# Optimization experiments

Measured on AMD Instinct MI355X. Metric: run time of the kernel, lower is better.

Reference implementation:

```python
import jax, jax.numpy as jnp
import numpy as np

B, N, DEG = 8, 8192, 16
E = B * N * DEG
K1 = 2458  # ceil(0.3*8192)
K2 = 738   # ceil(0.3*2458)
NUM_CLASSES = 10


def gat(x, src, dst, emask, W, a_s, a_d, bias):
    # PyG GATConv with add_self_loops=True, negative_slope=0.2, concat heads
    n = x.shape[0]
    H, F = a_s.shape
    xp = (x @ W).reshape(n, H, F)                      # [n,H,F]
    al_s = (xp * a_s).sum(-1)                          # [n,H]
    al_d = (xp * a_d).sum(-1)
    loops = jnp.arange(n, dtype=src.dtype)
    s2 = jnp.concatenate([src, loops])
    d2 = jnp.concatenate([dst, loops])
    m2 = jnp.concatenate([emask, jnp.ones(n, bool)])
    e = jax.nn.leaky_relu(al_s[s2] + al_d[d2], 0.2)    # [E+n,H]
    e = jnp.where(m2[:, None], e, -1e9)
    emax = jax.ops.segment_max(e, d2, num_segments=n)
    ex = jnp.where(m2[:, None], jnp.exp(e - emax[d2]), 0.0)
    den = jax.ops.segment_sum(ex, d2, num_segments=n)
    msg = ex[:, :, None] * xp[s2]                      # [E+n,H,F]
    out = jax.ops.segment_sum(msg, d2, num_segments=n) / den[:, :, None]
    return out.reshape(n, H * F) + bias


def inorm(x):
    # PyG InstanceNorm (affine=False): per-graph per-channel normalization
    xb = x.reshape(B, -1, x.shape[-1])
    mu = xb.mean(1, keepdims=True)
    var = ((xb - mu) ** 2).mean(1, keepdims=True)
    return ((xb - mu) / jnp.sqrt(var + 1e-5)).reshape(x.shape)


def topk_pool(x, src, dst, emask, p, k):
    # TopKPooling: score = tanh(x.p/|p|), keep top-k per graph, scale x by score
    n_tot = x.shape[0]
    n = n_tot // B
    score = jnp.tanh((x @ p) / jnp.linalg.norm(p))
    sv, si = jax.lax.top_k(score.reshape(B, n), k)     # [B,k]
    xg = jnp.take_along_axis(x.reshape(B, n, -1), si[:, :, None], axis=1)
    xnew = (xg * sv[:, :, None]).reshape(B * k, -1)
    perm = (si + (jnp.arange(B) * n)[:, None]).reshape(-1)
    newid = jnp.full(n_tot, -1, dtype=src.dtype).at[perm].set(
        jnp.arange(B * k, dtype=src.dtype))
    ns, nd = newid[src], newid[dst]
    m = emask & (ns >= 0) & (nd >= 0)
    return xnew, jnp.maximum(ns, 0), jnp.maximum(nd, 0), m


def setup_inputs() -> dict:
    key = jax.random.key(0)
    ks = jax.random.split(key, 32)
    pos = jax.random.normal(ks[0], (B * N, 3), jnp.float32)
    offs = jnp.repeat(jnp.arange(B, dtype=jnp.int32) * N, N * DEG)
    src = jax.random.randint(ks[1], (E,), 0, N, jnp.int32) + offs
    dst = jax.random.randint(ks[2], (E,), 0, N, jnp.int32) + offs

    def lin(k, fi, fo):
        return jax.random.normal(k, (fi, fo), jnp.float32) * (1.0 / np.sqrt(fi))

    d = dict(pos=pos, src=src, dst=dst)
    d['W1'] = lin(ks[3], 3, 32);   d['a_s1'] = jax.random.normal(ks[4], (2, 16)) * 0.2
    d['a_d1'] = jax.random.normal(ks[5], (2, 16)) * 0.2
    d['b1'] = jnp.zeros((32,));    d['p1'] = jax.random.normal(ks[6], (32,))
    d['W2'] = lin(ks[7], 32, 128); d['a_s2'] = jax.random.normal(ks[8], (2, 64)) * 0.2
    d['a_d2'] = jax.random.normal(ks[9], (2, 64)) * 0.2
    d['b2'] = jnp.zeros((128,));   d['p2'] = jax.random.normal(ks[10], (128,))
    d['W3'] = lin(ks[11], 128, 256); d['a_s3'] = jax.random.normal(ks[12], (1, 256)) * 0.1
    d['a_d3'] = jax.random.normal(ks[13], (1, 256)) * 0.1
    d['b3'] = jnp.zeros((256,))
    d['gw1'] = lin(ks[14], 256, 64);  d['gb1'] = jnp.zeros((64,))
    d['gw2'] = lin(ks[15], 64, 1);    d['gb2'] = jnp.zeros((1,))
    d['aw'] = lin(ks[16], 256, 256);  d['ab'] = jnp.zeros((256,))
    d['w1'] = lin(ks[17], 256, 512);  d['bb1'] = jnp.zeros((512,))
    d['w2'] = lin(ks[18], 512, 128);  d['bb2'] = jnp.zeros((128,))
    d['w3'] = lin(ks[19], 128, NUM_CLASSES); d['bb3'] = jnp.zeros((NUM_CLASSES,))
    return d


def reference(pos, src, dst, W1, a_s1, a_d1, b1, p1, W2, a_s2, a_d2, b2, p2,
              W3, a_s3, a_d3, b3, gw1, gb1, gw2, gb2, aw, ab,
              w1, bb1, w2, bb2, w3, bb3):
    emask = jnp.ones(src.shape[0], bool)
    x = gat(pos, src, dst, emask, W1, a_s1, a_d1, b1)
    x = jax.nn.elu(inorm(x))
    x, src, dst, emask = topk_pool(x, src, dst, emask, p1, K1)
    x = gat(x, src, dst, emask, W2, a_s2, a_d2, b2)
    x = jax.nn.elu(inorm(x))
    x, src, dst, emask = topk_pool(x, src, dst, emask, p2, K2)
    x = gat(x, src, dst, emask, W3, a_s3, a_d3, b3)
    x = jax.nn.elu(inorm(x))
    # GlobalAttention: gate_nn = Linear(256,64)+ELU+Linear(64,1); nn = Linear+ELU
    gate = jax.nn.elu(x @ gw1 + gb1) @ gw2 + gb2       # [M,1]
    h = jax.nn.elu(x @ aw + ab)                        # [M,256]
    a = jax.nn.softmax(gate.reshape(B, K2, 1), axis=1)
    g = (a * h.reshape(B, K2, 256)).sum(1)             # [B,256]
    z = jax.nn.elu(g @ w1 + bb1)   # dropout inactive in eval
    z = jax.nn.elu(z @ w2 + bb2)
    z = z @ w3 + bb3
    return jax.nn.log_softmax(z, axis=1)
```

## Files before the change

### kernel.cpp

```cpp
#include <hip/hip_runtime.h>
#include <cstdint>
#include <cstddef>

#define DI __device__ __forceinline__

namespace pk {

constexpr int NB1 = 65536;
constexpr int NE  = 1048576;
constexpr int BG  = 8;
constexpr int NPG1 = 8192;
constexpr int EPG1 = NE/BG;
constexpr int KP1 = 2458;
constexpr int KP2 = 738;
constexpr int NN2 = BG*KP1;
constexpr int NN3 = BG*KP2;
constexpr int REG2 = 16384;
constexpr int REG3 = 4096;
constexpr int CAP2 = BG*REG2;
constexpr int CAP3 = BG*REG3;
constexpr int CPB1 = 16;
constexpr int NTILE = 32;
constexpr int BKT = 5120;

DI float lrelu(float x){ return x > 0.f ? x : 0.2f*x; }
DI float eluf(float x){ return x > 0.f ? x : expf(x) - 1.f; }

DI int swz_block(){
  int nb = gridDim.x, b = blockIdx.x;
  if((nb & 7) == 0) return (b & 7)*(nb >> 3) + (b >> 3);
  return b;
}

__global__ __launch_bounds__(1024) void k_s1_front(
    const float* __restrict__ pos, const float* __restrict__ W,
    const float* __restrict__ as_, const float* __restrict__ ad_,
    float* __restrict__ xp, float* __restrict__ als, float* __restrict__ ald,
    const int* __restrict__ se, const int* __restrict__ de,
    int* __restrict__ part, int* __restrict__ bcur, int* __restrict__ bpk){
  __shared__ int h[NPG1];
  __shared__ int hbase[NTILE];
  __shared__ int hc[NTILE];
  int tid = threadIdx.x;
  if(blockIdx.x < 64){
    int i = blockIdx.x*1024 + tid;
    float p0=pos[3*i], p1=pos[3*i+1], p2=pos[3*i+2];
    float row[32];
#pragma unroll
    for(int c=0;c<32;c++) row[c] = p0*W[c] + p1*W[32+c] + p2*W[64+c];
    float s0=0.f,d0=0.f,s1=0.f,d1=0.f;
#pragma unroll
    for(int f=0;f<16;f++){
      s0 += row[f]*as_[f];        d0 += row[f]*ad_[f];
      s1 += row[16+f]*as_[16+f];  d1 += row[16+f]*ad_[16+f];
    }
    float4* o = reinterpret_cast<float4*>(xp + (size_t)i*32);
#pragma unroll
    for(int q=0;q<8;q++) o[q] = make_float4(row[4*q],row[4*q+1],row[4*q+2],row[4*q+3]);
    als[2*i]=s0; als[2*i+1]=s1; ald[2*i]=d0; ald[2*i+1]=d1;
    return;
  }
  int bb = blockIdx.x - 64;
  int g = bb & 7, t = bb >> 3;
  for(int i=tid;i<NPG1;i+=1024) h[i]=0;
  __syncthreads();
  const int4* de4 = (const int4*)(de + g*EPG1 + t*(EPG1/CPB1));
  const int4* se4 = (const int4*)(se + g*EPG1 + t*(EPG1/CPB1));
  int lo = g*NPG1;
  int4 dv[2], sv[2];
#pragma unroll
  for(int j=0;j<2;j++){ dv[j]=de4[j*1024+tid]; sv[j]=se4[j*1024+tid]; }
  int dl[8], sl[8];
#pragma unroll
  for(int j=0;j<2;j++){
    dl[4*j+0]=dv[j].x-lo; dl[4*j+1]=dv[j].y-lo; dl[4*j+2]=dv[j].z-lo; dl[4*j+3]=dv[j].w-lo;
    sl[4*j+0]=sv[j].x-lo; sl[4*j+1]=sv[j].y-lo; sl[4*j+2]=sv[j].z-lo; sl[4*j+3]=sv[j].w-lo;
  }
#pragma unroll
  for(int q=0;q<8;q++) atomicAdd(&h[dl[q]],1);
  __syncthreads();
  if(tid < NTILE){
    int ssum = 0;
    for(int i=0;i<256;i++) ssum += h[tid*256+i];
    hbase[tid] = atomicAdd(&bcur[g*NTILE+tid], ssum);
    hc[tid] = 0;
  }
  int* pp = part + (size_t)(g*CPB1+t)*NPG1;
  for(int i=tid;i<NPG1;i+=1024) pp[i]=h[i];
  __syncthreads();
#pragma unroll
  for(int q=0;q<8;q++){
    int tt = dl[q] >> 8;
    int p = atomicAdd(&hc[tt],1) + hbase[tt];
    bpk[(size_t)(g*NTILE+tt)*BKT + p] = (sl[q]<<13) | dl[q];
  }
}

__global__ __launch_bounds__(1024) void k_scan1(
    const int* __restrict__ part, int* __restrict__ cnt,
    int* __restrict__ rowptr){
  __shared__ int wsum[16];
  int g = blockIdx.x;
  int tid = threadIdx.x, lane = tid & 63, w = tid >> 6;
  constexpr int PER = NPG1/1024;
  int base = g*NPG1;
  int i0 = tid*PER;
  int v[PER]; int s = 0;
#pragma unroll
  for(int j=0;j<PER;j++){
    int i = i0+j;
    int x = 0;
#pragma unroll
    for(int p=0;p<CPB1;p++) x += part[(size_t)(g*CPB1+p)*NPG1 + i];
    cnt[base+i] = x;
    v[j] = s; s += x;
  }
  int inc = s;
  for(int o=1;o<64;o<<=1){ int t2=__shfl_up(inc,o,64); if(lane>=o) inc+=t2; }
  if(lane==63) wsum[w]=inc;
  __syncthreads();
  int wb=0;
  for(int k=0;k<w;k++) wb+=wsum[k];
  int tb = g*EPG1 + wb + inc - s;
#pragma unroll
  for(int j=0;j<PER;j++) rowptr[base+i0+j] = tb + v[j];
}

__global__ __launch_bounds__(1024) void k_scatter_b(
    const int* __restrict__ bcur, const int* __restrict__ bpk,
    const int* __restrict__ rowptr, int* __restrict__ eo){
  __shared__ int cur[256];
  int tid = threadIdx.x;
  int g = blockIdx.x & 7, t = blockIdx.x >> 3;
  int lo = g*NPG1 + t*256;
  if(tid < 256) cur[tid] = rowptr[lo + tid];
  __syncthreads();
  int cnt = bcur[g*NTILE + t];
  const int* bp = bpk + (size_t)(g*NTILE + t)*BKT;
  for(int i=tid; i<cnt; i+=1024){
    int pk = bp[i];
    int dlo = pk & 8191;
    int slo = pk >> 13;
    int p = atomicAdd(&cur[dlo - t*256], 1);
    eo[p] = g*NPG1 + slo;
  }
}

__global__ __launch_bounds__(256) void k_scatter_r(
    const int* __restrict__ se, const int* __restrict__ de,
    const int* __restrict__ gcnt, int reg,
    int* __restrict__ cursor, int* __restrict__ eo){
  int i = swz_block()*256 + threadIdx.x;
  int g = i / reg, loc = i % reg;
  if(loc < gcnt[g]){
    int p = atomicAdd(&cursor[de[i]], 1);
    eo[p] = se[i];
  }
}

template<int PER>
DI void scan256(const int* __restrict__ cnt, int R, int estride,
                int* __restrict__ rowptr, int* __restrict__ cursor, int g){
  __shared__ int wsum[4];
  int tid = threadIdx.x, lane = tid & 63, w = tid >> 6;
  int base = g*R;
  int i0 = tid*PER;
  int v[PER]; int s = 0;
#pragma unroll
  for(int j=0;j<PER;j++){ int i=i0+j; int x=(i<R)?cnt[base+i]:0; v[j]=s; s+=x; }
  int inc = s;
  for(int o=1;o<64;o<<=1){ int t=__shfl_up(inc,o,64); if(lane>=o) inc+=t; }
  if(lane==63) wsum[w]=inc;
  __syncthreads();
  int wb=0;
  for(int k=0;k<w;k++) wb+=wsum[k];
  int tb = g*estride + wb + inc - s;
#pragma unroll
  for(int j=0;j<PER;j++){
    int i=i0+j;
    if(i<R){
      int e=tb+v[j];
      rowptr[base+i]=e;
      cursor[base+i]=e;
    }
  }
}

template<int PER>
__global__ __launch_bounds__(256) void k_scan_w(
    const int* __restrict__ cnt, int R, int estride,
    int* __restrict__ rowptr, int* __restrict__ cursor){
  scan256<PER>(cnt, R, estride, rowptr, cursor, (int)blockIdx.x);
}

DI float inorm_of(const float* accum, int gc, float R, float x){
  float s = accum[gc*2], sq = accum[gc*2+1];
  float mu = s / R;
  float var = fmaxf(sq/R - mu*mu, 0.f);
  return eluf((x-mu)*rsqrtf(var+1e-5f));
}

template<int H,int F,int EB>
__global__ __launch_bounds__(256) void k_gat_fused(
    const float* __restrict__ xp, const float* __restrict__ als,
    const float* __restrict__ ald, const int* __restrict__ rowptr,
    const int* __restrict__ cnt, const int* __restrict__ esrc,
    const float* __restrict__ bias, float* __restrict__ out,
    float* __restrict__ accum, int RPG, int bpg){
  constexpr int C = H*F, C4 = C/4;
  constexpr int NPB = 256/C4;
  __shared__ float psum[4][C], psq[4][C];
  int tid = threadIdx.x;
  int nl = tid / C4, p = tid % C4;
  int work = (blockIdx.x & 7)*(gridDim.x >> 3) + (blockIdx.x >> 3);
  int g = work / bpg, t = work - g*bpg;
  int loc = t*NPB + nl;
  int node = g*RPG + loc;
  int hh = (4*p)/F;
  const float4* xp4 = (const float4*)xp;
  float4 r = make_float4(0.f,0.f,0.f,0.f);
  bool valid = loc < RPG;
  if(valid){
    float dvh = ald[node*H+hh];
    float sw  = expf(lrelu(als[node*H+hh] + dvh));
    float4 xs = xp4[(size_t)node*C4 + p];
    float den = sw;
    float ax=sw*xs.x, ay=sw*xs.y, az=sw*xs.z, aw_=sw*xs.w;
    int r0  = rowptr[node];
    int deg = cnt[node];
    for(int j=0; j<deg; j+=EB){
      int idx[EB]; float wv[EB]; float4 v[EB];
#pragma unroll
      for(int q=0;q<EB;q++)
        idx[q] = (j+q < deg) ? esrc[r0+j+q] : node;
#pragma unroll
      for(int q=0;q<EB;q++)
        wv[q] = als[idx[q]*H+hh];
#pragma unroll
      for(int q=0;q<EB;q++)
        v[q] = xp4[(size_t)idx[q]*C4 + p];
#pragma unroll
      for(int q=0;q<EB;q++){
        float w = (j+q < deg) ? expf(lrelu(wv[q] + dvh)) : 0.f;
        den += w;
        ax += w*v[q].x; ay += w*v[q].y; az += w*v[q].z; aw_ += w*v[q].w;
      }
    }
    float inv = 1.f / den;
    float4 bv = ((const float4*)bias)[p];
    r.x=ax*inv+bv.x; r.y=ay*inv+bv.y; r.z=az*inv+bv.z; r.w=aw_*inv+bv.w;
    ((float4*)out)[(size_t)node*C4 + p] = r;
  }
  float sx=r.x, sy=r.y, sz=r.z, sw2=r.w;
  float qx=r.x*r.x, qy=r.y*r.y, qz=r.z*r.z, qw=r.w*r.w;
#pragma unroll
  for(int off=C4; off<64; off<<=1){
    sx += __shfl_down(sx, off, 64); sy += __shfl_down(sy, off, 64);
    sz += __shfl_down(sz, off, 64); sw2 += __shfl_down(sw2, off, 64);
    qx += __shfl_down(qx, off, 64); qy += __shfl_down(qy, off, 64);
    qz += __shfl_down(qz, off, 64); qw += __shfl_down(qw, off, 64);
  }
  int lane = tid & 63, w = tid >> 6;
  if(lane < C4){
    psum[w][4*lane+0]=sx; psum[w][4*lane+1]=sy;
    psum[w][4*lane+2]=sz; psum[w][4*lane+3]=sw2;
    psq[w][4*lane+0]=qx;  psq[w][4*lane+1]=qy;
    psq[w][4*lane+2]=qz;  psq[w][4*lane+3]=qw;
  }
  __syncthreads();
  if(tid < C){
    float ts = psum[0][tid]+psum[1][tid]+psum[2][tid]+psum[3][tid];
    float tq = psq[0][tid]+psq[1][tid]+psq[2][tid]+psq[3][tid];
    atomicAdd(&accum[(g*C+tid)*2],   ts);
    atomicAdd(&accum[(g*C+tid)*2+1], tq);
  }
}

template<int K,int CO,int NPG,int H,int CHUNK>
__global__ __launch_bounds__(256) void k_cpt_gemm(
    const int* __restrict__ se, const int* __restrict__ de,
    const int* __restrict__ gcnt_in, int fixed_in, int reg_in,
    const int* __restrict__ newid, int* __restrict__ gcnt_out,
    int* __restrict__ ons, int* __restrict__ ond, int reg_out,
    int* __restrict__ cnt, int ncomp,
    const float* __restrict__ X, const float* __restrict__ naccum, int nRPG,
    const int* __restrict__ oldid, const float* __restrict__ scale,
    const float* __restrict__ W, float* __restrict__ Y,
    const float* __restrict__ a_s, const float* __restrict__ a_d,
    float* __restrict__ als, float* __restrict__ ald, int n){
  constexpr int SUB = 256/CO;
  constexpr int NB = SUB*NPG;
  static_assert(NB*K <= 2*CHUNK, "xs must fit the union");
  __shared__ int sm[2*CHUNK];
  __shared__ int run, tbase;
  __shared__ float ps[4][NPG], pd[4][NPG];
  int tid = threadIdx.x;
  if((int)blockIdx.x < ncomp){
    int* s_a = sm;
    int* s_b = sm + CHUNK;
    if(tid == 0) run = 0;
    __syncthreads();
    int blk = blockIdx.x;
    int g = blk & 7, t = blk >> 3;
    int mg = gcnt_in ? gcnt_in[g] : fixed_in;
    if(mg > reg_in) mg = reg_in;
    int base_l = t*CHUNK;
    if(base_l < mg){
      const int4* de4 = (const int4*)(de + (size_t)g*reg_in + base_l);
      const int4* se4 = (const int4*)(se + (size_t)g*reg_in + base_l);
      int4 BD[CHUNK/1024], BS[CHUNK/1024];
#pragma unroll
      for(int j=0;j<CHUNK/1024;j++){ BD[j]=de4[j*256+tid]; BS[j]=se4[j*256+tid]; }
      int cl = 0;
#pragma unroll
      for(int j=0;j<CHUNK/1024;j++){
        int eb = base_l + (j*256+tid)*4;
        int dd[4]={BD[j].x,BD[j].y,BD[j].z,BD[j].w};
        int ss[4]={BS[j].x,BS[j].y,BS[j].z,BS[j].w};
#pragma unroll
        for(int q=0;q<4;q++){
          if(eb+q < mg){
            int a = newid[ss[q]], b = newid[dd[q]];
            if(a>=0 && b>=0){ cl++; atomicAdd(&cnt[b], 1); }
          }
        }
      }
      int p0 = 0;
      if(cl) p0 = atomicAdd(&run, cl);
#pragma unroll
      for(int j=0;j<CHUNK/1024;j++){
        int eb = base_l + (j*256+tid)*4;
        int dd[4]={BD[j].x,BD[j].y,BD[j].z,BD[j].w};
        int ss[4]={BS[j].x,BS[j].y,BS[j].z,BS[j].w};
#pragma unroll
        for(int q=0;q<4;q++){
          if(eb+q < mg){
            int a = newid[ss[q]], b = newid[dd[q]];
            if(a>=0 && b>=0){ s_a[p0]=a; s_b[p0]=b; p0++; }
          }
        }
      }
    }
    __syncthreads();
    int ns = run;
    if(tid==0) tbase = ns ? atomicAdd(&gcnt_out[blockIdx.x & 7], ns) : 0;
    __syncthreads();
    int tb = tbase;
    int g2 = blockIdx.x & 7;
    for(int j=tid; j<ns; j+=256){
      int s2 = tb + j;
      if(s2 < reg_out){ ons[(size_t)g2*reg_out+s2]=s_a[j]; ond[(size_t)g2*reg_out+s2]=s_b[j]; }
    }
    return;
  }
  float (*xs)[K] = reinterpret_cast<float(*)[K]>(sm);
  int c = tid % CO, sg = tid / CO;
  int n0 = ((int)blockIdx.x - ncomp) * NB;
  for(int idx=tid; idx<NB*K; idx+=256){
    int r = idx / K, k = idx % K;
    int row = n0 + r;
    float v = 0.f;
    if(row < n){
      int orow = oldid[row];
      int og = orow / nRPG;
      v = inorm_of(naccum, og*K + k, (float)nRPG, X[(size_t)orow*K + k]) * scale[row];
    }
    xs[r][k] = v;
  }
  __syncthreads();
  float acc[NPG];
#pragma unroll
  for(int q=0;q<NPG;q++) acc[q]=0.f;
  for(int k=0;k<K;k++){
    float wv = W[(size_t)k*CO + c];
#pragma unroll
    for(int q=0;q<NPG;q++) acc[q] += xs[sg*NPG+q][k]*wv;
  }
  float asc = a_s[c], adc = a_d[c];
  float vs[NPG], vd[NPG];
#pragma unroll
  for(int q=0;q<NPG;q++){
    int row = n0 + sg*NPG + q;
    if(row < n) Y[(size_t)row*CO + c] = acc[q];
    vs[q] = acc[q]*asc; vd[q] = acc[q]*adc;
  }
#pragma unroll
  for(int o=32;o>0;o>>=1){
#pragma unroll
    for(int q=0;q<NPG;q++){
      vs[q] += __shfl_down(vs[q], o, 64);
      vd[q] += __shfl_down(vd[q], o, 64);
    }
  }
  int lane = tid & 63, w = tid >> 6;
  if(H == 2){
    if(lane == 0){
      int sg_ = w >> 1, h = w & 1;
#pragma unroll
      for(int q=0;q<NPG;q++){
        int row = n0 + sg_*NPG + q;
        if(row < n){ als[row*2+h] = vs[q]; ald[row*2+h] = vd[q]; }
      }
    }
  } else {
    if(lane == 0){
#pragma unroll
      for(int q=0;q<NPG;q++){ ps[w][q]=vs[q]; pd[w][q]=vd[q]; }
    }
    __syncthreads();
    if(tid < NPG){
      float s=0.f, d=0.f;
      for(int ww=0;ww<4;ww++){ s+=ps[ww][tid]; d+=pd[ww][tid]; }
      int row = n0 + tid;
      if(row < n){ als[row]=s; ald[row]=d; }
    }
  }
}

template<int C>
__global__ __launch_bounds__(256) void k_inorm_score(
    const float* __restrict__ x, const float* __restrict__ accum,
    const float* __restrict__ p, int R, int total,
    float* __restrict__ score, unsigned* __restrict__ u){
  __shared__ float rvp[256], rpp[256];
  int tid = threadIdx.x;
  int i = blockIdx.x*256 + tid;
  int c = tid & (C-1);
  bool act = i < total;
  float v = 0.f, pv = 0.f;
  if(act){
    int g = i / (R*C);
    v = inorm_of(accum, g*C+c, (float)R, x[i]);
    pv = p[c];
  }
  rvp[tid] = v*pv; rpp[tid] = pv*pv;
  __syncthreads();
#pragma unroll
  for(int s2=C/2; s2>0; s2>>=1){
    if(c < s2){ rvp[tid]+=rvp[tid+s2]; rpp[tid]+=rpp[tid+s2]; }
    __syncthreads();
  }
  if(act && c==0){
    float sv = tanhf(rvp[tid]*rsqrtf(rpp[tid]));
    int row = i / C;
    score[row] = sv;
    unsigned bts = __float_as_uint(sv);
    u[row] = (bts & 0x80000000u) ? ~bts : (bts | 0x80000000u);
  }
}

__global__ __launch_bounds__(1024) void k_topk(
    const unsigned* __restrict__ u, const float* __restrict__ score,
    int R, int Ksel, int* __restrict__ newid, int* __restrict__ oldid,
    float* __restrict__ scale){
  __shared__ int hist[2048];
  __shared__ int seg[32];
  __shared__ int sh_b, sh_k;
  __shared__ int wsA[16], wsB[16];
  __shared__ int carr0, carr1;
  int g = blockIdx.x, tid = threadIdx.x, lane = tid&63, w = tid>>6;
  const unsigned* ug = u + (size_t)g*R;
  unsigned prefix = 0;
  int K = Ksel;
  for(int lev=0; lev<3; lev++){
    int shf = (lev==0)?21:((lev==1)?10:0);
    int nb  = (lev==2)?1024:2048;
    for(int i=tid;i<2048;i+=1024) hist[i]=0;
    __syncthreads();
    for(int i=tid;i<R;i+=1024){
      unsigned v = ug[i];
      bool ok = (lev==0) || (lev==1 && (v>>21)==prefix) || (lev==2 && (v>>10)==prefix);
      if(ok) atomicAdd(&hist[(v>>shf)&(nb-1)], 1);
    }
    __syncthreads();
    int W = nb/32;
    if(tid<32){ int s=0; int lo=nb-W*(tid+1); for(int b=lo;b<lo+W;b++) s+=hist[b]; seg[tid]=s; }
    __syncthreads();
    if(tid==0){
      int kk=K, sgi=0;
      while(seg[sgi]<kk){ kk-=seg[sgi]; sgi++; }
      int b = nb-1-W*sgi;
      while(hist[b]<kk){ kk-=hist[b]; b--; }
      sh_b=b; sh_k=kk;
    }
    __syncthreads();
    int b = sh_b; K = sh_k;
    if(lev==0) prefix = (unsigned)b;
    else if(lev==1) prefix = (prefix<<11) | (unsigned)b;
    else prefix = (prefix<<10) | (unsigned)b;
    __syncthreads();
  }
  unsigned thr = prefix;
  int need = K;
  if(tid==0){ carr0=0; carr1=0; }
  __syncthreads();
  for(int bb=0; bb<R; bb+=1024){
    int i = bb + tid; bool in = i < R;
    unsigned uv = in ? ug[i] : 0u;
    int eq = (in && uv==thr) ? 1:0;
    int gt = (in && uv>thr) ? 1:0;
    int inc = eq;
    for(int o=1;o<64;o<<=1){ int t=__shfl_up(inc,o,64); if(lane>=o) inc+=t; }
    if(lane==63) wsA[w]=inc;
    __syncthreads();
    int wb=0; for(int k=0;k<w;k++) wb+=wsA[k];
    int eq_excl = carr0 + wb + inc - eq;
    int take = (gt || (eq && eq_excl<need)) ? 1 : 0;
    int inc2 = take;
    for(int o=1;o<64;o<<=1){ int t=__shfl_up(inc2,o,64); if(lane>=o) inc2+=t; }
    if(lane==63) wsB[w]=inc2;
    __syncthreads();
    int wb2=0; for(int k=0;k<w;k++) wb2+=wsB[k];
    int pos = carr1 + wb2 + inc2 - take;
    if(take){
      int nr = g*Ksel + pos;
      newid[(size_t)g*R+i] = nr;
      oldid[nr] = g*R+i;
      scale[nr] = score[(size_t)g*R+i];
    }
    __syncthreads();
    if(tid==1023){ carr0 += wb + inc; carr1 += wb2 + inc2; }
    __syncthreads();
  }
}

__global__ __launch_bounds__(256) void k_gate_fused(
    const float* __restrict__ X, const float* __restrict__ accum,
    const float* __restrict__ gw1, const float* __restrict__ gb1,
    const float* __restrict__ gw2, const float* __restrict__ gb2,
    float* __restrict__ gatev, int n){
  __shared__ float xs[8][256];
  int tid = threadIdx.x;
  int n0 = blockIdx.x*8;
  for(int idx=tid; idx<2048; idx+=256){
    int r = idx >> 8, k = idx & 255;
    int row = n0 + r;
    float v = 0.f;
    if(row < n){
      int g = row / KP2;
      v = inorm_of(accum, g*256+k, (float)KP2, X[(size_t)row*256 + k]);
    }
    xs[r][k] = v;
  }
  __syncthreads();
  int sg = tid >> 6, c = tid & 63;
  float a0 = 0.f, a1 = 0.f;
#pragma unroll 8
  for(int k=0;k<256;k++){
    float w = gw1[k*64+c];
    a0 = fmaf(xs[sg][k],   w, a0);
    a1 = fmaf(xs[sg+4][k], w, a1);
  }
  float gb = gb1[c], g2 = gw2[c];
  float v0 = eluf(a0 + gb) * g2;
  float v1 = eluf(a1 + gb) * g2;
#pragma unroll
  for(int o=32;o>0;o>>=1){
    v0 += __shfl_down(v0, o, 64);
    v1 += __shfl_down(v1, o, 64);
  }
  if(c==0){
    int r0 = n0 + sg, r1 = n0 + sg + 4;
    if(r0 < n) gatev[r0] = v0 + gb2[0];
    if(r1 < n) gatev[r1] = v1 + gb2[0];
  }
}

__global__ __launch_bounds__(256) void k_attn_gemm(
    const float* __restrict__ X, const float* __restrict__ accum,
    const float* __restrict__ W, const float* __restrict__ bias,
    const float* __restrict__ gatev, float* __restrict__ gvec){
  __shared__ float xs[8][256];
  __shared__ float red[256];
  int tid = threadIdx.x;
  int t = blockIdx.x, g = blockIdx.y;
  int r0 = t*8;
  float mx = -1e30f;
  for(int r=tid;r<KP2;r+=256) mx = fmaxf(mx, gatev[g*KP2+r]);
  red[tid]=mx; __syncthreads();
  for(int s=128;s>0;s>>=1){ if(tid<s) red[tid]=fmaxf(red[tid],red[tid+s]); __syncthreads(); }
  mx = red[0]; __syncthreads();
  float sm=0.f;
  for(int r=tid;r<KP2;r+=256) sm += expf(gatev[g*KP2+r]-mx);
  red[tid]=sm; __syncthreads();
  for(int s=128;s>0;s>>=1){ if(tid<s) red[tid]+=red[tid+s]; __syncthreads(); }
  float inv = 1.f/red[0];
  __syncthreads();
  for(int idx=tid; idx<2048; idx+=256){
    int r = idx >> 8, k = idx & 255;
    int lr = r0 + r;
    float v = 0.f;
    if(lr < KP2){
      int row = g*KP2 + lr;
      v = inorm_of(accum, g*256+k, (float)KP2, X[(size_t)row*256 + k]);
    }
    xs[r][k] = v;
  }
  __syncthreads();
  int c = tid;
  float acc[8];
#pragma unroll
  for(int q=0;q<8;q++) acc[q]=0.f;
  for(int k=0;k<256;k++){
    float wv = W[(size_t)k*256 + c];
#pragma unroll
    for(int q=0;q<8;q++) acc[q] += xs[q][k]*wv;
  }
  float bv = bias[c];
  float tot = 0.f;
#pragma unroll
  for(int q=0;q<8;q++){
    int lr = r0 + q;
    if(lr < KP2){
      float h = eluf(acc[q] + bv);
      tot += expf(gatev[g*KP2+lr]-mx) * h;
    }
  }
  atomicAdd(&gvec[g*256+c], tot*inv);
}

template<int K,int CO,int ACT>
__global__ __launch_bounds__(256) void k_mlp_t(
    const float* __restrict__ X, const float* __restrict__ W,
    const float* __restrict__ b, float* __restrict__ Y, int n){
  int i = blockIdx.x*256+threadIdx.x;
  if(i>=n*CO) return;
  int r=i/CO, c=i%CO;
  const float* xr = X + (size_t)r*K;
  float a=0.f;
#pragma unroll 16
  for(int k=0;k<K;k++) a = fmaf(xr[k], W[(size_t)k*CO+c], a);
  a += b[c];
  if(ACT) a = eluf(a);
  Y[i]=a;
}

__global__ __launch_bounds__(64) void k_head(
    const float* __restrict__ z2, const float* __restrict__ w3,
    const float* __restrict__ b3, float* __restrict__ out){
  __shared__ float zc[10]; __shared__ float mred, sred;
  int g=blockIdx.x, tid=threadIdx.x;
  if(tid<10){
    float a=0.f;
#pragma unroll 16
    for(int k=0;k<128;k++) a += z2[g*128+k]*w3[k*10+tid];
    zc[tid]=a+b3[tid];
  }
  __syncthreads();
  if(tid==0){
    float m=zc[0];
    for(int k=1;k<10;k++) m=fmaxf(m,zc[k]);
    float s=0.f;
    for(int k=0;k<10;k++) s+=expf(zc[k]-m);
    mred=m; sred=logf(s);
  }
  __syncthreads();
  if(tid<10) out[g*10+tid]=zc[tid]-mred-sred;
}

}

extern "C" void kernel_launch(void* const* d_in, const int* in_sizes, int n_in,
                              void* d_out, int out_size, void* d_ws, size_t ws_size,
                              hipStream_t stream){
  using namespace pk;
  (void)in_sizes; (void)n_in; (void)out_size;
  const float* pos = (const float*)d_in[0];
  const int*   src = (const int*)d_in[1];
  const int*   dst = (const int*)d_in[2];
  const float* W1  = (const float*)d_in[3];
  const float* as1 = (const float*)d_in[4];
  const float* ad1 = (const float*)d_in[5];
  const float* b1  = (const float*)d_in[6];
  const float* p1  = (const float*)d_in[7];
  const float* W2  = (const float*)d_in[8];
  const float* as2 = (const float*)d_in[9];
  const float* ad2 = (const float*)d_in[10];
  const float* b2  = (const float*)d_in[11];
  const float* p2  = (const float*)d_in[12];
  const float* W3  = (const float*)d_in[13];
  const float* as3 = (const float*)d_in[14];
  const float* ad3 = (const float*)d_in[15];
  const float* b3  = (const float*)d_in[16];
  const float* gw1 = (const float*)d_in[17];
  const float* gb1 = (const float*)d_in[18];
  const float* gw2 = (const float*)d_in[19];
  const float* gb2 = (const float*)d_in[20];
  const float* aw  = (const float*)d_in[21];
  const float* ab  = (const float*)d_in[22];
  const float* w1  = (const float*)d_in[23];
  const float* bb1 = (const float*)d_in[24];
  const float* w2  = (const float*)d_in[25];
  const float* bb2 = (const float*)d_in[26];
  const float* w3  = (const float*)d_in[27];
  const float* bb3 = (const float*)d_in[28];
  float* out = (float*)d_out;

  char* base = (char*)d_ws; size_t off = 0;
  auto alloc = [&](size_t nbytes)->char*{
    char* p = base + off; off = (off + nbytes + 255) & ~(size_t)255; return p;
  };
  int*   cnt2  = (int*)alloc((size_t)NN2*4);
  int*   cnt3  = (int*)alloc((size_t)NN3*4);
  int*   ecnt2 = (int*)alloc((size_t)BG*4);
  int*   ecnt3 = (int*)alloc((size_t)BG*4);
  float* acc1  = (float*)alloc((size_t)BG*32*2*4);
  float* acc2  = (float*)alloc((size_t)BG*128*2*4);
  float* acc3  = (float*)alloc((size_t)BG*256*2*4);
  float* gvec  = (float*)alloc((size_t)BG*256*4);
  int*   bcur1 = (int*)alloc((size_t)BG*NTILE*4);
  size_t zend = off;
  int*   newid1 = (int*)alloc((size_t)NB1*4);
  int*   newid2 = (int*)alloc((size_t)NN2*4);
  size_t fstart = (size_t)((char*)newid1 - base);
  size_t fend = off;
  int*      part1  = (int*)alloc((size_t)BG*CPB1*NPG1*4);
  int*      cnt1   = (int*)alloc((size_t)NB1*4);
  int*      bpk1   = (int*)alloc((size_t)BG*NTILE*BKT*4);
  float*    xp1    = (float*)alloc((size_t)NB1*32*4);
  float*    als1   = (float*)alloc((size_t)NB1*2*4);
  float*    ald1   = (float*)alloc((size_t)NB1*2*4);
  int*      rowptr1= (int*)alloc((size_t)NB1*4);
  int*      esrc1  = (int*)alloc((size_t)NE*4);
  float*    out1   = (float*)alloc((size_t)NB1*32*4);
  float*    score1 = (float*)alloc((size_t)NB1*4);
  unsigned* u1     = (unsigned*)alloc((size_t)NB1*4);
  int*      oldid1 = (int*)alloc((size_t)NN2*4);
  float*    scale1 = (float*)alloc((size_t)NN2*4);
  int*      ns2    = (int*)alloc((size_t)CAP2*4);
  int*      nd2    = (int*)alloc((size_t)CAP2*4);
  int*      rowptr2= (int*)alloc((size_t)NN2*4);
  int*      cursor2= (int*)alloc((size_t)NN2*4);
  int*      esrc2  = (int*)alloc((size_t)CAP2*4);
  float*    xp2    = (float*)alloc((size_t)NN2*128*4);
  float*    als2   = (float*)alloc((size_t)NN2*2*4);
  float*    ald2   = (float*)alloc((size_t)NN2*2*4);
  float*    out2   = (float*)alloc((size_t)NN2*128*4);
  float*    score2 = (float*)alloc((size_t)NN2*4);
  unsigned* u2     = (unsigned*)alloc((size_t)NN2*4);
  int*      oldid2 = (int*)alloc((size_t)NN3*4);
  float*    scale2 = (float*)alloc((size_t)NN3*4);
  int*      ns3    = (int*)alloc((size_t)CAP3*4);
  int*      nd3    = (int*)alloc((size_t)CAP3*4);
  int*      rowptr3= (int*)alloc((size_t)NN3*4);
  int*      cursor3= (int*)alloc((size_t)NN3*4);
  int*      esrc3  = (int*)alloc((size_t)CAP3*4);
  float*    xp3    = (float*)alloc((size_t)NN3*256*4);
  float*    als3   = (float*)alloc((size_t)NN3*4);
  float*    ald3   = (float*)alloc((size_t)NN3*4);
  float*    out3   = (float*)alloc((size_t)NN3*256*4);
  float*    gatev  = (float*)alloc((size_t)NN3*4);
  float*    z1     = (float*)alloc((size_t)BG*512*4);
  float*    z2     = (float*)alloc((size_t)BG*128*4);
  if(off > ws_size) return;

  auto cdiv = [](int a, int b){ return (a+b-1)/b; };

  hipMemsetAsync(base, 0, zend, stream);
  hipMemsetAsync(base + fstart, 0xFF, fend - fstart, stream);

  k_s1_front<<<192,1024,0,stream>>>(pos,W1,as1,ad1,xp1,als1,ald1,src,dst,part1,bcur1,bpk1);
  k_scan1<<<BG,1024,0,stream>>>(part1,cnt1,rowptr1);
  k_scatter_b<<<256,1024,0,stream>>>(bcur1,bpk1,rowptr1,esrc1);
  k_gat_fused<2,16,16><<<2048,256,0,stream>>>(xp1,als1,ald1,rowptr1,cnt1,esrc1,b1,out1,acc1,NPG1,256);
  k_inorm_score<32><<<cdiv(NB1*32,256),256,0,stream>>>(out1,acc1,p1,8192,NB1*32,score1,u1);
  k_topk<<<BG,1024,0,stream>>>(u1,score1,8192,KP1,newid1,oldid1,scale1);
  k_cpt_gemm<32,128,4,2,2048><<<512+cdiv(NN2,8),256,0,stream>>>(
      src,dst,nullptr,EPG1,EPG1,newid1,ecnt2,ns2,nd2,REG2,cnt2,512,
      out1,acc1,NPG1,oldid1,scale1,W2,xp2,as2,ad2,als2,ald2,NN2);
  k_scan_w<10><<<BG,256,0,stream>>>(cnt2,KP1,REG2,rowptr2,cursor2);
  k_scatter_r<<<CAP2/256,256,0,stream>>>(ns2,nd2,ecnt2,REG2,cursor2,esrc2);
  k_gat_fused<2,64,8><<<8*308,256,0,stream>>>(xp2,als2,ald2,rowptr2,cnt2,esrc2,b2,out2,acc2,KP1,308);
  k_inorm_score<128><<<cdiv(NN2*128,256),256,0,stream>>>(out2,acc2,p2,KP1,NN2*128,score2,u2);
  k_topk<<<BG,1024,0,stream>>>(u2,score2,KP1,KP2,newid2,oldid2,scale2);
  k_cpt_gemm<128,256,4,1,2048><<<64+cdiv(NN3,4),256,0,stream>>>(
      ns2,nd2,ecnt2,0,REG2,newid2,ecnt3,ns3,nd3,REG3,cnt3,64,
      out2,acc2,KP1,oldid2,scale2,W3,xp3,as3,ad3,als3,ald3,NN3);
  k_scan_w<3><<<BG,256,0,stream>>>(cnt3,KP2,REG3,rowptr3,cursor3);
  k_scatter_r<<<CAP3/256,256,0,stream>>>(ns3,nd3,ecnt3,REG3,cursor3,esrc3);
  k_gat_fused<1,256,4><<<8*185,256,0,stream>>>(xp3,als3,ald3,rowptr3,cnt3,esrc3,b3,out3,acc3,KP2,185);
  k_gate_fused<<<cdiv(NN3,8),256,0,stream>>>(out3,acc3,gw1,gb1,gw2,gb2,gatev,NN3);
  k_attn_gemm<<<dim3(cdiv(KP2,8),BG),256,0,stream>>>(out3,acc3,aw,ab,gatev,gvec);
  k_mlp_t<256,512,1><<<cdiv(BG*512,256),256,0,stream>>>(gvec,w1,bb1,z1,BG);
  k_mlp_t<512,128,1><<<cdiv(BG*128,256),256,0,stream>>>(z1,w2,bb2,z2,BG);
  k_head<<<BG,64,0,stream>>>(z2,w3,bb3,out);
}
```

Baseline: 395.3 us.

## Fold stage-1 CSR scan into bucket scatter and use shuffle reductions in score kernel

Drops the per-chunk partial histogram writes from the front kernel and removes the separate k_scan1 kernel. Each bucket-scatter block now builds its own 256-node histogram from its packed bucket, scans it, and derives the bucket base from a prefix over the bcur tile counts. This removes one launch and about 4MB of partial-count traffic, at the cost of reading the bucket twice. The inorm-score kernel also replaces its shared-memory tree reduction with wavefront shuffles, plus a two-wave combine when C is 128.

```diff
diff --git a/kernel.cpp b/kernel.cpp
--- a/kernel.cpp
+++ b/kernel.cpp
@@ -37,7 +37,7 @@
     const float* __restrict__ as_, const float* __restrict__ ad_,
     float* __restrict__ xp, float* __restrict__ als, float* __restrict__ ald,
     const int* __restrict__ se, const int* __restrict__ de,
-    int* __restrict__ part, int* __restrict__ bcur, int* __restrict__ bpk){
+    int* __restrict__ bcur, int* __restrict__ bpk){
   __shared__ int h[NPG1];
   __shared__ int hbase[NTILE];
   __shared__ int hc[NTILE];
@@ -85,8 +85,6 @@
     hbase[tid] = atomicAdd(&bcur[g*NTILE+tid], ssum);
     hc[tid] = 0;
   }
-  int* pp = part + (size_t)(g*CPB1+t)*NPG1;
-  for(int i=tid;i<NPG1;i+=1024) pp[i]=h[i];
   __syncthreads();
 #pragma unroll
   for(int q=0;q<8;q++){
@@ -96,53 +94,50 @@
   }
 }
 
-__global__ __launch_bounds__(1024) void k_scan1(
-    const int* __restrict__ part, int* __restrict__ cnt,
-    int* __restrict__ rowptr){
-  __shared__ int wsum[16];
-  int g = blockIdx.x;
-  int tid = threadIdx.x, lane = tid & 63, w = tid >> 6;
-  constexpr int PER = NPG1/1024;
-  int base = g*NPG1;
-  int i0 = tid*PER;
-  int v[PER]; int s = 0;
-#pragma unroll
-  for(int j=0;j<PER;j++){
-    int i = i0+j;
-    int x = 0;
-#pragma unroll
-    for(int p=0;p<CPB1;p++) x += part[(size_t)(g*CPB1+p)*NPG1 + i];
-    cnt[base+i] = x;
-    v[j] = s; s += x;
-  }
-  int inc = s;
-  for(int o=1;o<64;o<<=1){ int t2=__shfl_up(inc,o,64); if(lane>=o) inc+=t2; }
-  if(lane==63) wsum[w]=inc;
-  __syncthreads();
-  int wb=0;
-  for(int k=0;k<w;k++) wb+=wsum[k];
-  int tb = g*EPG1 + wb + inc - s;
-#pragma unroll
-  for(int j=0;j<PER;j++) rowptr[base+i0+j] = tb + v[j];
-}
-
 __global__ __launch_bounds__(1024) void k_scatter_b(
     const int* __restrict__ bcur, const int* __restrict__ bpk,
-    const int* __restrict__ rowptr, int* __restrict__ eo){
-  __shared__ int cur[256];
+    int* __restrict__ cnt, int* __restrict__ rowptr, int* __restrict__ eo){
+  __shared__ int hist[256], cur[256];
+  __shared__ int wsum[4];
+  __shared__ int sbase;
   int tid = threadIdx.x;
   int g = blockIdx.x & 7, t = blockIdx.x >> 3;
   int lo = g*NPG1 + t*256;
-  if(tid < 256) cur[tid] = rowptr[lo + tid];
-  __syncthreads();
-  int cnt = bcur[g*NTILE + t];
+  if(tid < 256) hist[tid] = 0;
+  if(tid < 32){
+    int v = bcur[g*NTILE + tid];
+    int inc = v;
+    for(int o=1;o<32;o<<=1){ int t2=__shfl_up(inc,o,64); if(tid>=o) inc+=t2; }
+    if(tid == t) sbase = g*EPG1 + inc - v;
+  }
+  __syncthreads();
+  int total = bcur[g*NTILE + t];
+  int base = sbase;
   const int* bp = bpk + (size_t)(g*NTILE + t)*BKT;
-  for(int i=tid; i<cnt; i+=1024){
+  for(int i=tid; i<total; i+=1024)
+    atomicAdd(&hist[(bp[i] & 8191) - t*256], 1);
+  __syncthreads();
+  int lane = tid & 63, w = tid >> 6;
+  int v = 0, inc = 0;
+  if(tid < 256){
+    v = hist[tid]; inc = v;
+    for(int o=1;o<64;o<<=1){ int t2=__shfl_up(inc,o,64); if(lane>=o) inc+=t2; }
+    if(lane==63) wsum[w]=inc;
+  }
+  __syncthreads();
+  if(tid < 256){
+    int wb=0;
+    for(int k=0;k<w;k++) wb+=wsum[k];
+    int e = base + wb + inc - v;
+    cnt[lo+tid] = v;
+    rowptr[lo+tid] = e;
+    cur[tid] = e;
+  }
+  __syncthreads();
+  for(int i=tid; i<total; i+=1024){
     int pk = bp[i];
-    int dlo = pk & 8191;
-    int slo = pk >> 13;
-    int p = atomicAdd(&cur[dlo - t*256], 1);
-    eo[p] = g*NPG1 + slo;
+    int p = atomicAdd(&cur[(pk & 8191) - t*256], 1);
+    eo[p] = g*NPG1 + (pk >> 13);
   }
 }
 
@@ -422,7 +417,6 @@
     const float* __restrict__ x, const float* __restrict__ accum,
     const float* __restrict__ p, int R, int total,
     float* __restrict__ score, unsigned* __restrict__ u){
-  __shared__ float rvp[256], rpp[256];
   int tid = threadIdx.x;
   int i = blockIdx.x*256 + tid;
   int c = tid & (C-1);
@@ -433,19 +427,38 @@
     v = inorm_of(accum, g*C+c, (float)R, x[i]);
     pv = p[c];
   }
-  rvp[tid] = v*pv; rpp[tid] = pv*pv;
-  __syncthreads();
-#pragma unroll
-  for(int s2=C/2; s2>0; s2>>=1){
-    if(c < s2){ rvp[tid]+=rvp[tid+s2]; rpp[tid]+=rpp[tid+s2]; }
-    __syncthreads();
-  }
-  if(act && c==0){
-    float sv = tanhf(rvp[tid]*rsqrtf(rpp[tid]));
-    int row = i / C;
-    score[row] = sv;
-    unsigned bts = __float_as_uint(sv);
-    u[row] = (bts & 0x80000000u) ? ~bts : (bts | 0x80000000u);
+  float vp = v*pv, pp = pv*pv;
+  if(C <= 64){
+#pragma unroll
+    for(int o=C/2;o>0;o>>=1){
+      vp += __shfl_down(vp, o, C);
+      pp += __shfl_down(pp, o, C);
+    }
+    if(act && c==0){
+      float sv = tanhf(vp*rsqrtf(pp));
+      int row = i / C;
+      score[row] = sv;
+      unsigned bts = __float_as_uint(sv);
+      u[row] = (bts & 0x80000000u) ? ~bts : (bts | 0x80000000u);
+    }
+  } else {
+    __shared__ float sv_[4], sp_[4];
+#pragma unroll
+    for(int o=32;o>0;o>>=1){
+      vp += __shfl_down(vp, o, 64);
+      pp += __shfl_down(pp, o, 64);
+    }
+    int lane = tid & 63, w = tid >> 6;
+    if(lane==0){ sv_[w]=vp; sp_[w]=pp; }
+    __syncthreads();
+    if(act && c==0){
+      float tv = sv_[w]+sv_[w+1], tp = sp_[w]+sp_[w+1];
+      float sv = tanhf(tv*rsqrtf(tp));
+      int row = i / C;
+      score[row] = sv;
+      unsigned bts = __float_as_uint(sv);
+      u[row] = (bts & 0x80000000u) ? ~bts : (bts | 0x80000000u);
+    }
   }
 }
 
@@ -714,7 +727,6 @@
   int*   newid2 = (int*)alloc((size_t)NN2*4);
   size_t fstart = (size_t)((char*)newid1 - base);
   size_t fend = off;
-  int*      part1  = (int*)alloc((size_t)BG*CPB1*NPG1*4);
   int*      cnt1   = (int*)alloc((size_t)NB1*4);
   int*      bpk1   = (int*)alloc((size_t)BG*NTILE*BKT*4);
   float*    xp1    = (float*)alloc((size_t)NB1*32*4);
@@ -759,9 +771,8 @@
   hipMemsetAsync(base, 0, zend, stream);
   hipMemsetAsync(base + fstart, 0xFF, fend - fstart, stream);
 
-  k_s1_front<<<192,1024,0,stream>>>(pos,W1,as1,ad1,xp1,als1,ald1,src,dst,part1,bcur1,bpk1);
-  k_scan1<<<BG,1024,0,stream>>>(part1,cnt1,rowptr1);
-  k_scatter_b<<<256,1024,0,stream>>>(bcur1,bpk1,rowptr1,esrc1);
+  k_s1_front<<<192,1024,0,stream>>>(pos,W1,as1,ad1,xp1,als1,ald1,src,dst,bcur1,bpk1);
+  k_scatter_b<<<256,1024,0,stream>>>(bcur1,bpk1,cnt1,rowptr1,esrc1);
   k_gat_fused<2,16,16><<<2048,256,0,stream>>>(xp1,als1,ald1,rowptr1,cnt1,esrc1,b1,out1,acc1,NPG1,256);
   k_inorm_score<32><<<cdiv(NB1*32,256),256,0,stream>>>(out1,acc1,p1,8192,NB1*32,score1,u1);
   k_topk<<<BG,1024,0,stream>>>(u1,score1,8192,KP1,newid1,oldid1,scale1);
```

Result: no change. 391.8 us (-0.9%).
